# Kernel optimization log

Hardware: AMD Instinct MI355X
Metric: run time of the kernel (lower is better)

## Reference

```python
import jax, jax.numpy as jnp
import numpy as np

MODEL_DIM = 768
NUM_HEADS = 12
HEAD_DIM = MODEL_DIM // NUM_HEADS
TEMPERATURE = 1.0


def setup_inputs() -> dict:
    key = jax.random.key(0)
    ks = jax.random.split(key, 14)
    B, S, M, D = 4, 2048, 512, MODEL_DIM
    scale = 0.02
    return {
        "query_hidden_states": jax.random.normal(ks[0], (B, S, D), jnp.float32),
        "memory_embeddings": jax.random.normal(ks[1], (B, M, D), jnp.float32),
        "memory_scores": jax.random.normal(ks[2], (B, M), jnp.float32),
        "Wq": jax.random.normal(ks[3], (D, D), jnp.float32) * scale,
        "bq": jnp.zeros((D,), jnp.float32),
        "Wk": jax.random.normal(ks[4], (D, D), jnp.float32) * scale,
        "bk": jnp.zeros((D,), jnp.float32),
        "Wv": jax.random.normal(ks[5], (D, D), jnp.float32) * scale,
        "bv": jnp.zeros((D,), jnp.float32),
        "Wo": jax.random.normal(ks[6], (D, D), jnp.float32) * scale,
        "bo": jnp.zeros((D,), jnp.float32),
        "Wg": jax.random.normal(ks[7], (2 * D, D), jnp.float32) * scale,
        "bg": jnp.zeros((D,), jnp.float32),
    }


def reference(query_hidden_states, memory_embeddings, memory_scores,
              Wq, bq, Wk, bk, Wv, bv, Wo, bo, Wg, bg):
    B, S, D = query_hidden_states.shape
    M = memory_embeddings.shape[1]
    H, Hd = NUM_HEADS, HEAD_DIM

    q = query_hidden_states @ Wq + bq            # [B,S,D]
    k = memory_embeddings @ Wk + bk              # [B,M,D]
    v = memory_embeddings @ Wv + bv              # [B,M,D]

    q = q.reshape(B, S, H, Hd).transpose(0, 2, 1, 3) / jnp.sqrt(jnp.float32(Hd))
    k = k.reshape(B, M, H, Hd).transpose(0, 2, 1, 3)
    v = v.reshape(B, M, H, Hd).transpose(0, 2, 1, 3)

    scores = jnp.einsum('bhsd,bhmd->bhsm', q, k) / TEMPERATURE
    # additive memory-score bias broadcast over heads and query positions
    scores = scores + memory_scores[:, None, None, :]
    attn = jax.nn.softmax(scores, axis=-1)       # [B,H,S,M]

    out = jnp.einsum('bhsm,bhmd->bhsd', attn, v)
    out = out.transpose(0, 2, 1, 3).reshape(B, S, D)
    out = out @ Wo + bo                          # [B,S,D]

    concat = jnp.concatenate([query_hidden_states, out], axis=-1)  # [B,S,2D]
    gate = jax.nn.sigmoid(concat @ Wg + bg)
    return gate * out + (1.0 - gate) * query_hidden_states
```

## Files before the change

kernel.cpp:

```cpp
#include <hip/hip_runtime.h>
#include <hip/hip_bf16.h>

#define DEV static __device__ __forceinline__

typedef __attribute__((ext_vector_type(4))) float f32x4;
typedef __attribute__((ext_vector_type(8))) short bf16x8;

DEV unsigned short f2bf(float f) {
  __hip_bfloat16 h = __float2bfloat16(f);
  union { __hip_bfloat16 h; unsigned short u; } v; v.h = h;
  return v.u;
}
DEV float bf2f(unsigned short u) {
  union { unsigned u; float f; } v; v.u = ((unsigned)u) << 16;
  return v.f;
}
DEV void gl_lds16(const unsigned short* g, unsigned short* l) {
  __builtin_amdgcn_global_load_lds(
      (const __attribute__((address_space(1))) void*)g,
      (__attribute__((address_space(3))) void*)l, 16, 0, 0);
}

struct T6 {
  const float* src[6];
  unsigned short* dst[6];
  int ldd[6];
};
__global__ void k_prep(const float* __restrict__ q, unsigned short* __restrict__ concat,
                       const float* __restrict__ mem, unsigned short* __restrict__ mem_bf,
                       T6 d) {
  __shared__ float tile[32][33];
  const int bid = blockIdx.x;
  if (bid < 7680) {
    const int i = bid * 256 + threadIdx.x;
    union { unsigned short u[4]; uint2 p; } o;
    if (i < 6144 * 256) {
      const int idx = i * 4;
      const int r = idx / 768, c = idx - r * 768;
      const float4 v = *(const float4*)(q + idx);
      o.u[0] = f2bf(v.x); o.u[1] = f2bf(v.y); o.u[2] = f2bf(v.z); o.u[3] = f2bf(v.w);
      *(uint2*)(concat + (size_t)r * 1536 + c) = o.p;
    } else {
      const int idx = (i - 6144 * 256) * 4;
      const float4 v = *(const float4*)(mem + idx);
      o.u[0] = f2bf(v.x); o.u[1] = f2bf(v.y); o.u[2] = f2bf(v.z); o.u[3] = f2bf(v.w);
      *(uint2*)(mem_bf + idx) = o.p;
    }
    return;
  }
  const int tb = bid - 7680;
  const int z = tb / 576, rem = tb - z * 576;
  const float* src = d.src[z];
  unsigned short* dst = d.dst[z];
  const int ldd = d.ldd[z];
  const int n0 = (rem % 24) * 32, k0 = (rem / 24) * 32;
  const int tx = threadIdx.x & 31, ty = threadIdx.x >> 5;
#pragma unroll
  for (int i = 0; i < 4; i++)
    tile[ty + i * 8][tx] = src[(size_t)(k0 + ty + i * 8) * 768 + n0 + tx];
  __syncthreads();
#pragma unroll
  for (int i = 0; i < 4; i++)
    dst[(size_t)(n0 + ty + i * 8) * ldd + k0 + tx] = f2bf(tile[tx][ty + i * 8]);
}

#define GEMM_STAGE(Aptr, lda, Bptr, ldb, buf, k0)                            \
  {                                                                          \
    _Pragma("unroll") for (int p = 0; p < 4; p++) {                          \
      const int ch = p * 256 + t;                                            \
      const int row = ch >> 3, s = ch & 7;                                   \
      gl_lds16(Aptr + (size_t)(r0 + row) * lda + (k0) + ((s ^ (row & 7)) * 8), \
               &Al[buf][ch * 8]);                                            \
    }                                                                        \
    _Pragma("unroll") for (int p = 0; p < 2; p++) {                          \
      const int ch = p * 256 + t;                                            \
      const int row = ch >> 3, s = ch & 7;                                   \
      gl_lds16(Bptr + (size_t)(c0 + row) * ldb + (k0) + ((s ^ (row & 7)) * 8), \
               &Bl[buf][ch * 8]);                                            \
    }                                                                        \
  }

#define GEMM_COMPUTE(cur)                                                    \
  _Pragma("unroll") for (int kb = 0; kb < 2; kb++) {                         \
    bf16x8 af[4], bfr[2];                                                    \
    _Pragma("unroll") for (int mi = 0; mi < 4; mi++) {                       \
      const int r = wr * 64 + mi * 16 + l15;                                 \
      const int s = (kb * 4 + l4) ^ (r & 7);                                 \
      af[mi] = *(const bf16x8*)&Al[cur][r * 64 + s * 8];                     \
    }                                                                        \
    _Pragma("unroll") for (int ni = 0; ni < 2; ni++) {                       \
      const int r = wc * 32 + ni * 16 + l15;                                 \
      const int s = (kb * 4 + l4) ^ (r & 7);                                 \
      bfr[ni] = *(const bf16x8*)&Bl[cur][r * 64 + s * 8];                    \
    }                                                                        \
    _Pragma("unroll") for (int mi = 0; mi < 4; mi++)                         \
      _Pragma("unroll") for (int ni = 0; ni < 2; ni++)                       \
        acc[mi][ni] = __builtin_amdgcn_mfma_f32_16x16x32_bf16(               \
            af[mi], bfr[ni], acc[mi][ni], 0, 0, 0);                          \
  }

__global__ __launch_bounds__(256) void k_gemm_qkv(
    const unsigned short* __restrict__ concat,
    const unsigned short* __restrict__ mem_bf,
    const unsigned short* __restrict__ Wqt,
    const unsigned short* __restrict__ Wkvt,
    const float* __restrict__ bq, const float* __restrict__ bk,
    const float* __restrict__ bv,
    unsigned short* __restrict__ q_bf, unsigned short* __restrict__ k_bf,
    unsigned short* __restrict__ vT) {
  __shared__ alignas(16) unsigned short Al[2][128 * 64];
  __shared__ alignas(16) unsigned short Bl[2][64 * 64];
  const int t = threadIdx.x;
  const int cpx = gridDim.x >> 3;
  const int swz = (blockIdx.x & 7) * cpx + (blockIdx.x >> 3);
  const int role = swz < 768 ? 0 : 1;
  const int sub = role == 0 ? swz : swz - 768;
  const int gx = role == 0 ? 12 : 24;
  const int r0 = (sub / gx) * 128, c0 = (sub % gx) * 64;
  const unsigned short* A = role == 0 ? concat : mem_bf;
  const unsigned short* Bt = role == 0 ? Wqt : Wkvt;
  const int lda = role == 0 ? 1536 : 768;
  const int ldb = 768;
  const float scale = role == 0 ? 0.125f * 1.4426950408889634f : 1.f;
  const int lane = t & 63, l15 = lane & 15, l4 = lane >> 4;
  const int wid = t >> 6, wr = wid >> 1, wc = wid & 1;

  f32x4 acc[4][2];
#pragma unroll
  for (int mi = 0; mi < 4; mi++)
#pragma unroll
    for (int ni = 0; ni < 2; ni++) acc[mi][ni] = (f32x4){0.f, 0.f, 0.f, 0.f};

  GEMM_STAGE(A, lda, Bt, ldb, 0, 0);
  const int nt = 12;
  for (int tk = 0; tk < nt; ++tk) {
    const int cur = tk & 1;
    __syncthreads();
    if (tk + 1 < nt) GEMM_STAGE(A, lda, Bt, ldb, cur ^ 1, (tk + 1) * 64);
    GEMM_COMPUTE(cur);
  }

#pragma unroll
  for (int ni = 0; ni < 2; ni++) {
    const int c = c0 + wc * 32 + ni * 16 + l15;
    const float bvv = role == 0 ? bq[c] : (c < 768 ? bk[c] : bv[c - 768]);
#pragma unroll
    for (int mi = 0; mi < 4; mi++) {
      const int rbase = r0 + wr * 64 + mi * 16 + l4 * 4;
#pragma unroll
      for (int i = 0; i < 4; i++) {
        const int r = rbase + i;
        const float val = (acc[mi][ni][i] + bvv) * scale;
        if (role == 0) {
          q_bf[(size_t)r * 768 + c] = f2bf(val);
        } else if (c < 768) {
          k_bf[(size_t)r * 768 + c] = f2bf(val);
        } else {
          const int cc = c - 768;
          const int b = r >> 9, m = r & 511;
          const int h = cc >> 6, dd = cc & 63;
          vT[(((size_t)(b * 12 + h)) * 64 + dd) * 512 + m] = f2bf(val);
        }
      }
    }
  }
}

template <int EPI>
__global__ __launch_bounds__(256) void k_gemm(
    const unsigned short* __restrict__ A, int lda,
    const unsigned short* __restrict__ Bt, int ldb,
    const float* __restrict__ bias, int K, float scale,
    unsigned short* __restrict__ out0,
    const unsigned short* __restrict__ concat_in,
    const float* __restrict__ qy, float* __restrict__ dout, int gx) {
  __shared__ alignas(16) unsigned short Al[2][128 * 64];
  __shared__ alignas(16) unsigned short Bl[2][64 * 64];
  const int t = threadIdx.x;
  const int cpx = gridDim.x >> 3;
  const int swz = (blockIdx.x & 7) * cpx + (blockIdx.x >> 3);
  const int r0 = (swz / gx) * 128, c0 = (swz % gx) * 64;
  const int lane = t & 63, l15 = lane & 15, l4 = lane >> 4;
  const int wid = t >> 6, wr = wid >> 1, wc = wid & 1;

  f32x4 acc[4][2];
#pragma unroll
  for (int mi = 0; mi < 4; mi++)
#pragma unroll
    for (int ni = 0; ni < 2; ni++) acc[mi][ni] = (f32x4){0.f, 0.f, 0.f, 0.f};

  GEMM_STAGE(A, lda, Bt, ldb, 0, 0);
  const int nt = K >> 6;
  for (int tk = 0; tk < nt; ++tk) {
    const int cur = tk & 1;
    __syncthreads();
    if (tk + 1 < nt) GEMM_STAGE(A, lda, Bt, ldb, cur ^ 1, (tk + 1) * 64);
    GEMM_COMPUTE(cur);
  }

#pragma unroll
  for (int ni = 0; ni < 2; ni++) {
    const int c = c0 + wc * 32 + ni * 16 + l15;
    const float bvv = bias[c];
#pragma unroll
    for (int mi = 0; mi < 4; mi++) {
      const int rbase = r0 + wr * 64 + mi * 16 + l4 * 4;
#pragma unroll
      for (int i = 0; i < 4; i++) {
        const int r = rbase + i;
        const float val = acc[mi][ni][i] + bvv;
        if (EPI == 2) {
          out0[(size_t)r * 1536 + 768 + c] = f2bf(val);
        } else {
          const float g = 1.f / (1.f + __expf(-val));
          const float o = bf2f(concat_in[(size_t)r * 1536 + 768 + c]);
          const float q = qy[(size_t)r * 768 + c];
          dout[(size_t)r * 768 + c] = g * o + (1.f - g) * q;
        }
      }
    }
  }
}

__global__ __launch_bounds__(256, 3) void k_attn(
    const unsigned short* __restrict__ qbf,
    const unsigned short* __restrict__ kbf,
    const unsigned short* __restrict__ vT,
    const float* __restrict__ mscore,
    unsigned short* __restrict__ aout) {
  const int st = blockIdx.x, h = blockIdx.y, b = blockIdx.z;
  __shared__ float bias_s[512];
  __shared__ alignas(16) unsigned short Kl[2][64 * 64];
  __shared__ alignas(16) unsigned short Vl[2][64 * 64];
  __shared__ alignas(16) unsigned short P[4][16][72];
  const int t = threadIdx.x;
  const int wid = t >> 6, lane = t & 63, l15 = lane & 15, l4 = lane >> 4;
  for (int i = t; i < 512; i += 256)
    bias_s[i] = (mscore[b * 512 + i] - 10.0f) * 1.4426950408889634f;

  const int srow = st * 64 + wid * 16;
  const unsigned short* qrow = qbf + ((size_t)(b * 2048 + srow + l15)) * 768 + h * 64;
  bf16x8 qa[2];
  qa[0] = *(const bf16x8*)(qrow + l4 * 8);
  qa[1] = *(const bf16x8*)(qrow + 32 + l4 * 8);

  const unsigned short* kbase = kbf + (size_t)(b * 512) * 768 + h * 64;
  const unsigned short* vbase = vT + ((size_t)(b * 12 + h)) * 64 * 512;

#define STAGE_A(buf, m0_)                                                     \
  {                                                                           \
    _Pragma("unroll") for (int p = 0; p < 2; p++) {                           \
      const int chk = p * 256 + t;                                            \
      const int row = chk >> 3, s = chk & 7;                                  \
      gl_lds16(kbase + (size_t)((m0_) + row) * 768 + ((s ^ (row & 7)) * 8),   \
               &Kl[buf][chk * 8]);                                            \
    }                                                                         \
    _Pragma("unroll") for (int p = 0; p < 2; p++) {                           \
      const int chk = p * 256 + t;                                            \
      const int row = chk >> 3, s = chk & 7;                                  \
      gl_lds16(vbase + (size_t)row * 512 + (m0_) + ((s ^ (row & 7)) * 8),     \
               &Vl[buf][chk * 8]);                                            \
    }                                                                         \
  }

  f32x4 O[4];
#pragma unroll
  for (int dt = 0; dt < 4; dt++) O[dt] = (f32x4){0.f, 0.f, 0.f, 0.f};
  float rs[4] = {0.f, 0.f, 0.f, 0.f};

  STAGE_A(0, 0);
  for (int ch = 0; ch < 8; ++ch) {
    const int cur = ch & 1;
    __syncthreads();
    if (ch + 1 < 8) STAGE_A(cur ^ 1, (ch + 1) * 64);

    f32x4 s4[4];
#pragma unroll
    for (int tt = 0; tt < 4; tt++) {
      const float bs = bias_s[ch * 64 + tt * 16 + l15];
      s4[tt] = (f32x4){bs, bs, bs, bs};
    }
#pragma unroll
    for (int kb = 0; kb < 2; kb++)
#pragma unroll
      for (int tt = 0; tt < 4; tt++) {
        const int r = tt * 16 + l15;
        const bf16x8 bb = *(const bf16x8*)&Kl[cur][r * 64 + (((kb * 4 + l4) ^ (r & 7)) * 8)];
        s4[tt] = __builtin_amdgcn_mfma_f32_16x16x32_bf16(qa[kb], bb, s4[tt], 0, 0, 0);
      }

#pragma unroll
    for (int tt = 0; tt < 4; tt++)
#pragma unroll
      for (int i = 0; i < 4; i++) {
        const float p = exp2f(s4[tt][i]);
        rs[i] += p;
        P[wid][l4 * 4 + i][tt * 16 + l15] = f2bf(p);
      }

#pragma unroll
    for (int mk = 0; mk < 2; mk++) {
      const bf16x8 pa = *(const bf16x8*)&P[wid][l15][mk * 32 + l4 * 8];
#pragma unroll
      for (int dt = 0; dt < 4; dt++) {
        const int r = dt * 16 + l15;
        const bf16x8 vb = *(const bf16x8*)&Vl[cur][r * 64 + (((mk * 4 + l4) ^ (r & 7)) * 8)];
        O[dt] = __builtin_amdgcn_mfma_f32_16x16x32_bf16(pa, vb, O[dt], 0, 0, 0);
      }
    }
  }
#undef STAGE_A

#pragma unroll
  for (int d = 1; d < 16; d <<= 1)
#pragma unroll
    for (int i = 0; i < 4; i++) rs[i] += __shfl_xor(rs[i], d);
  float rinv[4];
#pragma unroll
  for (int i = 0; i < 4; i++) rinv[i] = 1.f / rs[i];
  const size_t rbase = (size_t)(b * 2048 + srow + l4 * 4);
#pragma unroll
  for (int dt = 0; dt < 4; dt++)
#pragma unroll
    for (int i = 0; i < 4; i++)
      aout[(rbase + i) * 768 + h * 64 + dt * 16 + l15] = f2bf(O[dt][i] * rinv[i]);
}

extern "C" void kernel_launch(void* const* d_in, const int* in_sizes, int n_in,
                              void* d_out, int out_size, void* d_ws, size_t ws_size,
                              hipStream_t stream) {
  const float* query  = (const float*)d_in[0];
  const float* memory = (const float*)d_in[1];
  const float* mscore = (const float*)d_in[2];
  const float* Wq = (const float*)d_in[3];
  const float* bq = (const float*)d_in[4];
  const float* Wk = (const float*)d_in[5];
  const float* bk = (const float*)d_in[6];
  const float* Wv = (const float*)d_in[7];
  const float* bv = (const float*)d_in[8];
  const float* Wo = (const float*)d_in[9];
  const float* bo = (const float*)d_in[10];
  const float* Wg = (const float*)d_in[11];
  const float* bg = (const float*)d_in[12];
  float* dout = (float*)d_out;

  char* ws = (char*)d_ws;
  unsigned short* concat = (unsigned short*)ws; ws += (size_t)8192 * 1536 * 2;
  unsigned short* mem_bf = (unsigned short*)ws; ws += (size_t)2048 * 768 * 2;
  unsigned short* Wqt = (unsigned short*)ws;    ws += (size_t)768 * 768 * 2;
  unsigned short* Wkvt = (unsigned short*)ws;   ws += (size_t)1536 * 768 * 2;
  unsigned short* Wot = (unsigned short*)ws;    ws += (size_t)768 * 768 * 2;
  unsigned short* Wgt = (unsigned short*)ws;    ws += (size_t)768 * 1536 * 2;
  unsigned short* q_bf = (unsigned short*)ws;   ws += (size_t)8192 * 768 * 2;
  unsigned short* k_bf = (unsigned short*)ws;   ws += (size_t)2048 * 768 * 2;
  unsigned short* vT = (unsigned short*)ws;     ws += (size_t)4 * 12 * 64 * 512 * 2;
  unsigned short* attn_bf = (unsigned short*)ws;

  T6 td;
  td.src[0] = Wq;  td.dst[0] = Wqt;              td.ldd[0] = 768;
  td.src[1] = Wk;  td.dst[1] = Wkvt;             td.ldd[1] = 768;
  td.src[2] = Wv;  td.dst[2] = Wkvt + 768 * 768; td.ldd[2] = 768;
  td.src[3] = Wo;  td.dst[3] = Wot;              td.ldd[3] = 768;
  td.src[4] = Wg;  td.dst[4] = Wgt;              td.ldd[4] = 1536;
  td.src[5] = Wg + 768 * 768; td.dst[5] = Wgt + 768; td.ldd[5] = 1536;
  k_prep<<<7680 + 3456, 256, 0, stream>>>(query, concat, memory, mem_bf, td);

  k_gemm_qkv<<<1152, 256, 0, stream>>>(concat, mem_bf, Wqt, Wkvt,
                                       bq, bk, bv, q_bf, k_bf, vT);
  k_attn<<<dim3(32, 12, 4), 256, 0, stream>>>(q_bf, k_bf, vT, mscore, attn_bf);
  k_gemm<2><<<64 * 12, 256, 0, stream>>>(attn_bf, 768, Wot, 768, bo, 768, 1.f,
                                         concat, nullptr, nullptr, nullptr, 12);
  k_gemm<3><<<64 * 12, 256, 0, stream>>>(concat, 1536, Wgt, 1536, bg, 1536, 1.f,
                                         nullptr, concat, query, dout, 12);
}
```

Before: 127.8 us.

## Triple-buffer GEMM LDS tiles with partial vmcnt waits to overlap loads

Replaces the double-buffered GEMM main loop with a three-stage LDS ring buffer that keeps two tiles in flight. It waits with s_waitcnt vmcnt(6) rather than draining all loads, and uses a raw s_barrier with sched_barriers in place of __syncthreads. The goal is to hide global-to-LDS load latency behind MFMA compute. In exchange LDS use per block rises from 48KB to 72KB, which may reduce blocks per CU, and correctness now depends on the hand-written vmcnt count matching the six loads issued per stage.

Result: slower. 154.0 us (+20.5%).

```diff
diff --git a/kernel.cpp b/kernel.cpp
--- a/kernel.cpp
+++ b/kernel.cpp
@@ -80,23 +80,44 @@
     }                                                                        \
   }
 
-#define GEMM_COMPUTE(cur)                                                    \
+#define GEMM_COMPUTE(b)                                                      \
   _Pragma("unroll") for (int kb = 0; kb < 2; kb++) {                         \
     bf16x8 af[4], bfr[2];                                                    \
     _Pragma("unroll") for (int mi = 0; mi < 4; mi++) {                       \
       const int r = wr * 64 + mi * 16 + l15;                                 \
       const int s = (kb * 4 + l4) ^ (r & 7);                                 \
-      af[mi] = *(const bf16x8*)&Al[cur][r * 64 + s * 8];                     \
+      af[mi] = *(const bf16x8*)&Al[b][r * 64 + s * 8];                       \
     }                                                                        \
     _Pragma("unroll") for (int ni = 0; ni < 2; ni++) {                       \
       const int r = wc * 32 + ni * 16 + l15;                                 \
       const int s = (kb * 4 + l4) ^ (r & 7);                                 \
-      bfr[ni] = *(const bf16x8*)&Bl[cur][r * 64 + s * 8];                    \
+      bfr[ni] = *(const bf16x8*)&Bl[b][r * 64 + s * 8];                      \
     }                                                                        \
     _Pragma("unroll") for (int mi = 0; mi < 4; mi++)                         \
       _Pragma("unroll") for (int ni = 0; ni < 2; ni++)                       \
         acc[mi][ni] = __builtin_amdgcn_mfma_f32_16x16x32_bf16(               \
             af[mi], bfr[ni], acc[mi][ni], 0, 0, 0);                          \
+  }
+
+#define GEMM_LOOP(Aptr, lda, Bptr, ldb, K)                                   \
+  {                                                                          \
+    const int nt = (K) >> 6;                                                 \
+    GEMM_STAGE(Aptr, lda, Bptr, ldb, 0, 0);                                  \
+    GEMM_STAGE(Aptr, lda, Bptr, ldb, 1, 64);                                 \
+    int b = 0;                                                               \
+    for (int tk = 0; tk < nt; ++tk) {                                        \
+      __builtin_amdgcn_sched_barrier(0);                                     \
+      if (tk < nt - 1) { asm volatile("s_waitcnt vmcnt(6)" ::: "memory"); }  \
+      else             { asm volatile("s_waitcnt vmcnt(0)" ::: "memory"); }  \
+      __builtin_amdgcn_s_barrier();                                          \
+      __builtin_amdgcn_sched_barrier(0);                                     \
+      if (tk + 2 < nt) {                                                     \
+        const int bn = b + 2 >= 3 ? b - 1 : b + 2;                           \
+        GEMM_STAGE(Aptr, lda, Bptr, ldb, bn, (tk + 2) * 64);                 \
+      }                                                                      \
+      GEMM_COMPUTE(b);                                                       \
+      b = b + 1 >= 3 ? 0 : b + 1;                                            \
+    }                                                                        \
   }
 
 __global__ __launch_bounds__(256) void k_gemm_qkv(
@@ -108,8 +129,8 @@
     const float* __restrict__ bv,
     unsigned short* __restrict__ q_bf, unsigned short* __restrict__ k_bf,
     unsigned short* __restrict__ vT) {
-  __shared__ alignas(16) unsigned short Al[2][128 * 64];
-  __shared__ alignas(16) unsigned short Bl[2][64 * 64];
+  __shared__ alignas(16) unsigned short Al[3][128 * 64];
+  __shared__ alignas(16) unsigned short Bl[3][64 * 64];
   const int t = threadIdx.x;
   const int cpx = gridDim.x >> 3;
   const int swz = (blockIdx.x & 7) * cpx + (blockIdx.x >> 3);
@@ -131,14 +152,7 @@
 #pragma unroll
     for (int ni = 0; ni < 2; ni++) acc[mi][ni] = (f32x4){0.f, 0.f, 0.f, 0.f};
 
-  GEMM_STAGE(A, lda, Bt, ldb, 0, 0);
-  const int nt = 12;
-  for (int tk = 0; tk < nt; ++tk) {
-    const int cur = tk & 1;
-    __syncthreads();
-    if (tk + 1 < nt) GEMM_STAGE(A, lda, Bt, ldb, cur ^ 1, (tk + 1) * 64);
-    GEMM_COMPUTE(cur);
-  }
+  GEMM_LOOP(A, lda, Bt, ldb, 768);
 
 #pragma unroll
   for (int ni = 0; ni < 2; ni++) {
@@ -174,8 +188,8 @@
     unsigned short* __restrict__ out0,
     const unsigned short* __restrict__ concat_in,
     const float* __restrict__ qy, float* __restrict__ dout, int gx) {
-  __shared__ alignas(16) unsigned short Al[2][128 * 64];
-  __shared__ alignas(16) unsigned short Bl[2][64 * 64];
+  __shared__ alignas(16) unsigned short Al[3][128 * 64];
+  __shared__ alignas(16) unsigned short Bl[3][64 * 64];
   const int t = threadIdx.x;
   const int cpx = gridDim.x >> 3;
   const int swz = (blockIdx.x & 7) * cpx + (blockIdx.x >> 3);
@@ -189,14 +203,7 @@
 #pragma unroll
     for (int ni = 0; ni < 2; ni++) acc[mi][ni] = (f32x4){0.f, 0.f, 0.f, 0.f};
 
-  GEMM_STAGE(A, lda, Bt, ldb, 0, 0);
-  const int nt = K >> 6;
-  for (int tk = 0; tk < nt; ++tk) {
-    const int cur = tk & 1;
-    __syncthreads();
-    if (tk + 1 < nt) GEMM_STAGE(A, lda, Bt, ldb, cur ^ 1, (tk + 1) * 64);
-    GEMM_COMPUTE(cur);
-  }
+  GEMM_LOOP(A, lda, Bt, ldb, K);
 
 #pragma unroll
   for (int ni = 0; ni < 2; ni++) {
```

## Replace LDS-staged GEMM mainloop with direct global-to-register MFMA operand loads

Applied to the files above, without the earlier changes.

Both GEMM kernels drop their shared-memory double buffer and the per-tile barriers. Each wave now loads its MFMA A and B fragments straight from global memory into registers, relying on L1/L2 for reuse. This removes the LDS traffic and the synchronisation, but operand reuse across waves is lost: global load volume rises, and latency is exposed with no explicit prefetch beyond the two-way unroll.

Result: slower. 293.1 us (+129.4%).

```diff
diff --git a/kernel.cpp b/kernel.cpp
--- a/kernel.cpp
+++ b/kernel.cpp
@@ -64,39 +64,25 @@
     dst[(size_t)(n0 + ty + i * 8) * ldd + k0 + tx] = f2bf(tile[tx][ty + i * 8]);
 }
 
-#define GEMM_STAGE(Aptr, lda, Bptr, ldb, buf, k0)                            \
+#define GEMM_DIRECT_LOOP(Aptr, lda, Bptr, ldb, K)                            \
   {                                                                          \
-    _Pragma("unroll") for (int p = 0; p < 4; p++) {                          \
-      const int ch = p * 256 + t;                                            \
-      const int row = ch >> 3, s = ch & 7;                                   \
-      gl_lds16(Aptr + (size_t)(r0 + row) * lda + (k0) + ((s ^ (row & 7)) * 8), \
-               &Al[buf][ch * 8]);                                            \
+    const unsigned short* Ap = (Aptr) + (size_t)(r0 + wr * 64 + l15) * (lda) + l4 * 8; \
+    const unsigned short* Bp = (Bptr) + (size_t)(c0 + wc * 32 + l15) * (ldb) + l4 * 8; \
+    const int nt = (K) >> 6;                                                 \
+    _Pragma("unroll 2") for (int tk = 0; tk < nt; ++tk) {                    \
+      bf16x8 af[4][2], bfr[2][2];                                            \
+      _Pragma("unroll") for (int mi = 0; mi < 4; mi++)                       \
+        _Pragma("unroll") for (int kb = 0; kb < 2; kb++)                     \
+          af[mi][kb] = *(const bf16x8*)(Ap + (size_t)(mi * 16) * (lda) + tk * 64 + kb * 32); \
+      _Pragma("unroll") for (int ni = 0; ni < 2; ni++)                       \
+        _Pragma("unroll") for (int kb = 0; kb < 2; kb++)                     \
+          bfr[ni][kb] = *(const bf16x8*)(Bp + (size_t)(ni * 16) * (ldb) + tk * 64 + kb * 32); \
+      _Pragma("unroll") for (int kb = 0; kb < 2; kb++)                       \
+        _Pragma("unroll") for (int mi = 0; mi < 4; mi++)                     \
+          _Pragma("unroll") for (int ni = 0; ni < 2; ni++)                   \
+            acc[mi][ni] = __builtin_amdgcn_mfma_f32_16x16x32_bf16(           \
+                af[mi][kb], bfr[ni][kb], acc[mi][ni], 0, 0, 0);              \
     }                                                                        \
-    _Pragma("unroll") for (int p = 0; p < 2; p++) {                          \
-      const int ch = p * 256 + t;                                            \
-      const int row = ch >> 3, s = ch & 7;                                   \
-      gl_lds16(Bptr + (size_t)(c0 + row) * ldb + (k0) + ((s ^ (row & 7)) * 8), \
-               &Bl[buf][ch * 8]);                                            \
-    }                                                                        \
-  }
-
-#define GEMM_COMPUTE(cur)                                                    \
-  _Pragma("unroll") for (int kb = 0; kb < 2; kb++) {                         \
-    bf16x8 af[4], bfr[2];                                                    \
-    _Pragma("unroll") for (int mi = 0; mi < 4; mi++) {                       \
-      const int r = wr * 64 + mi * 16 + l15;                                 \
-      const int s = (kb * 4 + l4) ^ (r & 7);                                 \
-      af[mi] = *(const bf16x8*)&Al[cur][r * 64 + s * 8];                     \
-    }                                                                        \
-    _Pragma("unroll") for (int ni = 0; ni < 2; ni++) {                       \
-      const int r = wc * 32 + ni * 16 + l15;                                 \
-      const int s = (kb * 4 + l4) ^ (r & 7);                                 \
-      bfr[ni] = *(const bf16x8*)&Bl[cur][r * 64 + s * 8];                    \
-    }                                                                        \
-    _Pragma("unroll") for (int mi = 0; mi < 4; mi++)                         \
-      _Pragma("unroll") for (int ni = 0; ni < 2; ni++)                       \
-        acc[mi][ni] = __builtin_amdgcn_mfma_f32_16x16x32_bf16(               \
-            af[mi], bfr[ni], acc[mi][ni], 0, 0, 0);                          \
   }
 
 __global__ __launch_bounds__(256) void k_gemm_qkv(
@@ -108,8 +94,6 @@
     const float* __restrict__ bv,
     unsigned short* __restrict__ q_bf, unsigned short* __restrict__ k_bf,
     unsigned short* __restrict__ vT) {
-  __shared__ alignas(16) unsigned short Al[2][128 * 64];
-  __shared__ alignas(16) unsigned short Bl[2][64 * 64];
   const int t = threadIdx.x;
   const int cpx = gridDim.x >> 3;
   const int swz = (blockIdx.x & 7) * cpx + (blockIdx.x >> 3);
@@ -120,7 +104,6 @@
   const unsigned short* A = role == 0 ? concat : mem_bf;
   const unsigned short* Bt = role == 0 ? Wqt : Wkvt;
   const int lda = role == 0 ? 1536 : 768;
-  const int ldb = 768;
   const float scale = role == 0 ? 0.125f * 1.4426950408889634f : 1.f;
   const int lane = t & 63, l15 = lane & 15, l4 = lane >> 4;
   const int wid = t >> 6, wr = wid >> 1, wc = wid & 1;
@@ -131,14 +114,7 @@
 #pragma unroll
     for (int ni = 0; ni < 2; ni++) acc[mi][ni] = (f32x4){0.f, 0.f, 0.f, 0.f};
 
-  GEMM_STAGE(A, lda, Bt, ldb, 0, 0);
-  const int nt = 12;
-  for (int tk = 0; tk < nt; ++tk) {
-    const int cur = tk & 1;
-    __syncthreads();
-    if (tk + 1 < nt) GEMM_STAGE(A, lda, Bt, ldb, cur ^ 1, (tk + 1) * 64);
-    GEMM_COMPUTE(cur);
-  }
+  GEMM_DIRECT_LOOP(A, lda, Bt, 768, 768);
 
 #pragma unroll
   for (int ni = 0; ni < 2; ni++) {
@@ -174,8 +150,6 @@
     unsigned short* __restrict__ out0,
     const unsigned short* __restrict__ concat_in,
     const float* __restrict__ qy, float* __restrict__ dout, int gx) {
-  __shared__ alignas(16) unsigned short Al[2][128 * 64];
-  __shared__ alignas(16) unsigned short Bl[2][64 * 64];
   const int t = threadIdx.x;
   const int cpx = gridDim.x >> 3;
   const int swz = (blockIdx.x & 7) * cpx + (blockIdx.x >> 3);
@@ -189,14 +163,7 @@
 #pragma unroll
     for (int ni = 0; ni < 2; ni++) acc[mi][ni] = (f32x4){0.f, 0.f, 0.f, 0.f};
 
-  GEMM_STAGE(A, lda, Bt, ldb, 0, 0);
-  const int nt = K >> 6;
-  for (int tk = 0; tk < nt; ++tk) {
-    const int cur = tk & 1;
-    __syncthreads();
-    if (tk + 1 < nt) GEMM_STAGE(A, lda, Bt, ldb, cur ^ 1, (tk + 1) * 64);
-    GEMM_COMPUTE(cur);
-  }
+  GEMM_DIRECT_LOOP(A, lda, Bt, ldb, K);
 
 #pragma unroll
   for (int ni = 0; ni < 2; ni++) {
```
